# Kernel tuning notes

Hardware: AMD Instinct MI355X
Metric: run time of the kernel (lower is better)

Reference implementation:

```python
import jax, jax.numpy as jnp
import numpy as np

BL = 5
N = 2 ** BL  # 32; LUT is (N+1) x (N+1)


def setup_inputs() -> dict:
    key = jax.random.key(0)
    k1, k2, k3 = jax.random.split(key, 3)
    M, K, O = 512, 256, 256
    x = jax.random.uniform(k1, (M, K), dtype=jnp.float32)              # activations in [0,1)
    W = jax.random.uniform(k2, (O, K), dtype=jnp.float32) * 2.0 - 1.0  # weights in [-1,1)
    b = jax.random.uniform(k3, (O,), dtype=jnp.float32) * 2.0 - 1.0
    # Stochastic-computing multiplication LUT: A[i, j] ~ i*j/N (floored), i,j in [0, N]
    i = np.arange(N + 1, dtype=np.float32)
    lut = jnp.asarray(np.floor(np.outer(i, i) / N), dtype=jnp.float32)
    return {"x": x, "W": W, "b": b, "lut": lut}


def _sanitize(t):
    t = jnp.where(jnp.isnan(t), jnp.zeros_like(t), t)
    return jnp.where(jnp.isinf(t), jnp.ones_like(t), t)


def sc_mat_mac_p(a, b, c, lut, n):
    # Faithful port of SC_MAT_MAC_p: quantize -> LUT gather over all (row, out) pairs ->
    # sign-correct -> reduce over K -> requantize -> add quantized bias -> rescale.
    a = _sanitize(a)
    b = _sanitize(b)
    c = _sanitize(c)
    amax = jnp.abs(a).max()
    amax = jnp.where(amax == 0, jnp.ones_like(amax), amax)
    dmax = jnp.maximum(jnp.abs(b).max(), jnp.abs(c).max())
    dmax = jnp.where(dmax == 0, jnp.ones_like(dmax), dmax)
    # SBL2 = int(log2(int(N / amax))); SN2 = 2**SBL2 (truncations match torch int())
    sn2 = 2.0 ** jnp.floor(jnp.log2(jnp.floor(n / amax)))
    sn1 = 2.0 ** jnp.floor(jnp.log2(jnp.floor(n / dmax)))
    aa = (a * sn2).astype(jnp.int32)  # [M, K], |aa| <= N
    bb = (b * sn1).astype(jnp.int32)  # [O, K], |bb| <= N
    cc = (c * sn1).astype(jnp.int32)  # [O]
    # LUT gather over the full cross product (original materializes this via
    # repeat_interleave/repeat; here it is a broadcasted gather of shape [M, O, K]).
    prod = lut[jnp.abs(aa)[:, None, :], jnp.abs(bb)[None, :, :]]          # [M, O, K]
    sgn = (jnp.sign(aa)[:, None, :] * jnp.sign(bb)[None, :, :]).astype(prod.dtype)
    x9 = (sgn * prod).sum(axis=-1)                                        # [M, O]
    d = (x9 / sn2).astype(jnp.int32) + cc[None, :]
    return d.astype(jnp.float32) / sn1


def reference(x, W, b, lut):
    # out = linear(x); out.data = SC_MAT_MAC_p(...)  -> value is the SC result,
    # gradient path is the dense linear (straight-through via .data assignment).
    lin = x @ W.T + b
    p = sc_mat_mac_p(x, W, b, lut, N)
    return lin + jax.lax.stop_gradient(p - lin)
```

## Files before the change

kernel.cpp:

```cpp
#include <hip/hip_runtime.h>
#include <stdint.h>


#define MROWS 512
#define KDIM  256
#define OCOLS 256
#define E2_GUESS 5
#define E1_GUESS 5

__device__ __forceinline__ void store_uc(unsigned int* p, unsigned int v) {
    asm volatile("global_store_dword %0, %1, off sc0 sc1"
                 :: "v"((unsigned long long)(uintptr_t)p), "v"(v) : "memory");
}
__device__ __forceinline__ unsigned int load_uc(const unsigned int* p) {
    unsigned int v;
    asm volatile("global_load_dword %0, %1, off sc0 sc1\n\t"
                 "s_waitcnt vmcnt(0)"
                 : "=v"(v) : "v"((unsigned long long)(uintptr_t)p) : "memory");
    return v;
}

__device__ __forceinline__ void get_scales(float amax, float dmax, int& e2, int& e1) {
    if (amax == 0.0f) amax = 1.0f;
    if (dmax == 0.0f) dmax = 1.0f;
    float q2 = 32.0f / amax;
    float q1 = 32.0f / dmax;
    int f2 = (q2 >= 1073741824.0f) ? 0x40000000 : (int)floorf(q2);
    int f1 = (q1 >= 1073741824.0f) ? 0x40000000 : (int)floorf(q1);
    if (f2 < 1) f2 = 1;
    if (f1 < 1) f1 = 1;
    e2 = 31 - __clz(f2);
    e1 = 31 - __clz(f1);
}

__device__ __forceinline__ float max4(float4 v) {
    return fmaxf(fmaxf(fabsf(v.x), fabsf(v.y)), fmaxf(fabsf(v.z), fabsf(v.w)));
}

__device__ __forceinline__ void quant_row(const float* __restrict__ x, int m, int o,
                                          float sn2f, unsigned int* a_sh) {
    if (o < KDIM / 4) {
        float4 xv = ((const float4*)(x + (size_t)m * KDIM))[o];
        int a0 = (int)(xv.x * sn2f) & 0xFF;
        int a1 = (int)(xv.y * sn2f) & 0xFF;
        int a2 = (int)(xv.z * sn2f) & 0xFF;
        int a3 = (int)(xv.w * sn2f) & 0xFF;
        a_sh[o] = (unsigned int)(a0 | (a1 << 8) | (a2 << 16) | (a3 << 24));
    }
}

__device__ __forceinline__ int mac_loop(const float* __restrict__ W, int o,
                                        const unsigned int* a_sh, float sn1f) {
    const float4* wrow = (const float4*)(W + (size_t)o * KDIM);
    int sum = 0;
    #pragma unroll 8
    for (int kk = 0; kk < KDIM / 4; ++kk) {
        float4 wv = wrow[kk];
        unsigned int ap = a_sh[kk];
        float wfv[4] = {wv.x, wv.y, wv.z, wv.w};
        #pragma unroll
        for (int j = 0; j < 4; ++j) {
            int bv = (int)(wfv[j] * sn1f);
            int av = ((int)(ap << (24 - 8 * j))) >> 24;
            int s  = av * bv;
            sum += (s + ((s >> 31) & 31)) >> 5;
        }
    }
    return sum;
}

__global__ __launch_bounds__(256, 2)
void k_one(unsigned int* __restrict__ wsp, const float* __restrict__ x,
           const float* __restrict__ W, const float* __restrict__ b,
           float* __restrict__ out) {
    __shared__ unsigned int a_sh[KDIM / 4];
    __shared__ float sm[8];
    __shared__ int s_e[2];

    const int m = blockIdx.x;
    const int o = threadIdx.x;
    const int wave = o >> 6;

    if (m < 64) {
        const float4* xf = (const float4*)x;
        const float4* wf = (const float4*)W;
        float va = fmaxf(max4(xf[m * 512 + o]), max4(xf[m * 512 + 256 + o]));
        float vd = max4(wf[m * 256 + o]);
        if (m == 0 && o < 64)
            vd = fmaxf(vd, max4(((const float4*)b)[o]));
        #pragma unroll
        for (int s = 32; s >= 1; s >>= 1) {
            va = fmaxf(va, __shfl_xor(va, s, 64));
            vd = fmaxf(vd, __shfl_xor(vd, s, 64));
        }
        if ((o & 63) == 0) { sm[2 * wave] = va; sm[2 * wave + 1] = vd; }
        __syncthreads();
        if (o == 0) {
            float a = fmaxf(fmaxf(sm[0], sm[2]), fmaxf(sm[4], sm[6]));
            float d = fmaxf(fmaxf(sm[1], sm[3]), fmaxf(sm[5], sm[7]));
            store_uc(&wsp[2 * m],     __float_as_uint(a));
            store_uc(&wsp[2 * m + 1], __float_as_uint(d));
        }
        __syncthreads();
    }

    float bo = b[o];
    quant_row(x, m, o, (float)(1 << E2_GUESS), a_sh);
    __syncthreads();
    int sum = mac_loop(W, o, a_sh, (float)(1 << E1_GUESS));

    if (wave == 0) {
        unsigned int w0, w1;
        bool all;
        do {
            w0 = load_uc(&wsp[2 * o]);
            w1 = load_uc(&wsp[2 * o + 1]);
            all = __all(((w0 | w1) & 0x80000000u) == 0u);
            if (!all) __builtin_amdgcn_s_sleep(1);
        } while (!all);
        float va = __uint_as_float(w0);
        float vd = __uint_as_float(w1);
        #pragma unroll
        for (int s = 32; s >= 1; s >>= 1) {
            va = fmaxf(va, __shfl_xor(va, s, 64));
            vd = fmaxf(vd, __shfl_xor(vd, s, 64));
        }
        if (o == 0) {
            int e2, e1;
            get_scales(va, vd, e2, e1);
            s_e[0] = e2; s_e[1] = e1;
        }
    }
    __syncthreads();

    const int e2 = s_e[0];
    const int e1 = s_e[1];

    if ((e2 != E2_GUESS) | (e1 != E1_GUESS)) {
        quant_row(x, m, o, (float)(1 << e2), a_sh);
        __syncthreads();
        sum = mac_loop(W, o, a_sh, (float)(1 << e1));
    }

    const float sn1f = (float)(1 << e1);
    int cc = (int)(bo * sn1f);
    int d  = ((sum + ((sum >> 31) & ((1 << e2) - 1))) >> e2) + cc;
    out[(size_t)m * OCOLS + o] = (float)d * (1.0f / sn1f);
}

extern "C" void kernel_launch(void* const* d_in, const int* in_sizes, int n_in,
                              void* d_out, int out_size, void* d_ws, size_t ws_size,
                              hipStream_t stream) {
    const float* x = (const float*)d_in[0];
    const float* W = (const float*)d_in[1];
    const float* b = (const float*)d_in[2];
    float* out = (float*)d_out;
    unsigned int* wsp = (unsigned int*)d_ws;

    k_one<<<MROWS, 256, 0, stream>>>(wsp, x, W, b, out);
}
```

Baseline: 74.71 us.

## Split fused kernel into separate scale-reduction and main MAC kernels

Replaces the single kernel, which spun on uncached workspace flags and speculatively ran the MAC with guessed scales, with two launches: a 64-block max-reduction kernel and a main kernel that reads the finished scales and runs the MAC once. This removes the cross-block spin-wait and the possible redundant recompute. It adds a second kernel launch and its launch gap, and drops the overlap of the speculative MAC with the reduction. The launch-bounds occupancy hint of 2 is also removed.

```diff
diff --git a/kernel.cpp b/kernel.cpp
--- a/kernel.cpp
+++ b/kernel.cpp
@@ -5,20 +5,6 @@
 #define MROWS 512
 #define KDIM  256
 #define OCOLS 256
-#define E2_GUESS 5
-#define E1_GUESS 5
-
-__device__ __forceinline__ void store_uc(unsigned int* p, unsigned int v) {
-    asm volatile("global_store_dword %0, %1, off sc0 sc1"
-                 :: "v"((unsigned long long)(uintptr_t)p), "v"(v) : "memory");
-}
-__device__ __forceinline__ unsigned int load_uc(const unsigned int* p) {
-    unsigned int v;
-    asm volatile("global_load_dword %0, %1, off sc0 sc1\n\t"
-                 "s_waitcnt vmcnt(0)"
-                 : "=v"(v) : "v"((unsigned long long)(uintptr_t)p) : "memory");
-    return v;
-}
 
 __device__ __forceinline__ void get_scales(float amax, float dmax, int& e2, int& e1) {
     if (amax == 0.0f) amax = 1.0f;
@@ -35,18 +21,6 @@
 
 __device__ __forceinline__ float max4(float4 v) {
     return fmaxf(fmaxf(fabsf(v.x), fabsf(v.y)), fmaxf(fabsf(v.z), fabsf(v.w)));
-}
-
-__device__ __forceinline__ void quant_row(const float* __restrict__ x, int m, int o,
-                                          float sn2f, unsigned int* a_sh) {
-    if (o < KDIM / 4) {
-        float4 xv = ((const float4*)(x + (size_t)m * KDIM))[o];
-        int a0 = (int)(xv.x * sn2f) & 0xFF;
-        int a1 = (int)(xv.y * sn2f) & 0xFF;
-        int a2 = (int)(xv.z * sn2f) & 0xFF;
-        int a3 = (int)(xv.w * sn2f) & 0xFF;
-        a_sh[o] = (unsigned int)(a0 | (a1 << 8) | (a2 << 16) | (a3 << 24));
-    }
 }
 
 __device__ __forceinline__ int mac_loop(const float* __restrict__ W, int o,
@@ -69,57 +43,53 @@
     return sum;
 }
 
-__global__ __launch_bounds__(256, 2)
-void k_one(unsigned int* __restrict__ wsp, const float* __restrict__ x,
-           const float* __restrict__ W, const float* __restrict__ b,
-           float* __restrict__ out) {
+__global__ __launch_bounds__(256)
+void k_scales(unsigned int* __restrict__ wsp, const float* __restrict__ x,
+              const float* __restrict__ W, const float* __restrict__ b) {
+    __shared__ float sm[8];
+    const int m = blockIdx.x;
+    const int o = threadIdx.x;
+    const int wave = o >> 6;
+
+    const float4* xf = (const float4*)x;
+    const float4* wf = (const float4*)W;
+    float va = fmaxf(max4(xf[m * 512 + o]), max4(xf[m * 512 + 256 + o]));
+    float vd = max4(wf[m * 256 + o]);
+    if (m == 0 && o < 64)
+        vd = fmaxf(vd, max4(((const float4*)b)[o]));
+    #pragma unroll
+    for (int s = 32; s >= 1; s >>= 1) {
+        va = fmaxf(va, __shfl_xor(va, s, 64));
+        vd = fmaxf(vd, __shfl_xor(vd, s, 64));
+    }
+    if ((o & 63) == 0) { sm[2 * wave] = va; sm[2 * wave + 1] = vd; }
+    __syncthreads();
+    if (o == 0) {
+        float a = fmaxf(fmaxf(sm[0], sm[2]), fmaxf(sm[4], sm[6]));
+        float d = fmaxf(fmaxf(sm[1], sm[3]), fmaxf(sm[5], sm[7]));
+        wsp[2 * m]     = __float_as_uint(a);
+        wsp[2 * m + 1] = __float_as_uint(d);
+    }
+}
+
+__global__ __launch_bounds__(256)
+void k_main(const unsigned int* __restrict__ wsp, const float* __restrict__ x,
+            const float* __restrict__ W, const float* __restrict__ b,
+            float* __restrict__ out) {
     __shared__ unsigned int a_sh[KDIM / 4];
-    __shared__ float sm[8];
     __shared__ int s_e[2];
 
     const int m = blockIdx.x;
     const int o = threadIdx.x;
-    const int wave = o >> 6;
-
-    if (m < 64) {
-        const float4* xf = (const float4*)x;
-        const float4* wf = (const float4*)W;
-        float va = fmaxf(max4(xf[m * 512 + o]), max4(xf[m * 512 + 256 + o]));
-        float vd = max4(wf[m * 256 + o]);
-        if (m == 0 && o < 64)
-            vd = fmaxf(vd, max4(((const float4*)b)[o]));
-        #pragma unroll
-        for (int s = 32; s >= 1; s >>= 1) {
-            va = fmaxf(va, __shfl_xor(va, s, 64));
-            vd = fmaxf(vd, __shfl_xor(vd, s, 64));
-        }
-        if ((o & 63) == 0) { sm[2 * wave] = va; sm[2 * wave + 1] = vd; }
-        __syncthreads();
-        if (o == 0) {
-            float a = fmaxf(fmaxf(sm[0], sm[2]), fmaxf(sm[4], sm[6]));
-            float d = fmaxf(fmaxf(sm[1], sm[3]), fmaxf(sm[5], sm[7]));
-            store_uc(&wsp[2 * m],     __float_as_uint(a));
-            store_uc(&wsp[2 * m + 1], __float_as_uint(d));
-        }
-        __syncthreads();
-    }
 
     float bo = b[o];
-    quant_row(x, m, o, (float)(1 << E2_GUESS), a_sh);
-    __syncthreads();
-    int sum = mac_loop(W, o, a_sh, (float)(1 << E1_GUESS));
+    float4 xv;
+    if (o < KDIM / 4)
+        xv = ((const float4*)(x + (size_t)m * KDIM))[o];
 
-    if (wave == 0) {
-        unsigned int w0, w1;
-        bool all;
-        do {
-            w0 = load_uc(&wsp[2 * o]);
-            w1 = load_uc(&wsp[2 * o + 1]);
-            all = __all(((w0 | w1) & 0x80000000u) == 0u);
-            if (!all) __builtin_amdgcn_s_sleep(1);
-        } while (!all);
-        float va = __uint_as_float(w0);
-        float vd = __uint_as_float(w1);
+    if (o < 64) {
+        float va = __uint_as_float(wsp[2 * o]);
+        float vd = __uint_as_float(wsp[2 * o + 1]);
         #pragma unroll
         for (int s = 32; s >= 1; s >>= 1) {
             va = fmaxf(va, __shfl_xor(va, s, 64));
@@ -135,14 +105,20 @@
 
     const int e2 = s_e[0];
     const int e1 = s_e[1];
+    const float sn2f = (float)(1 << e2);
+    const float sn1f = (float)(1 << e1);
 
-    if ((e2 != E2_GUESS) | (e1 != E1_GUESS)) {
-        quant_row(x, m, o, (float)(1 << e2), a_sh);
-        __syncthreads();
-        sum = mac_loop(W, o, a_sh, (float)(1 << e1));
+    if (o < KDIM / 4) {
+        int a0 = (int)(xv.x * sn2f) & 0xFF;
+        int a1 = (int)(xv.y * sn2f) & 0xFF;
+        int a2 = (int)(xv.z * sn2f) & 0xFF;
+        int a3 = (int)(xv.w * sn2f) & 0xFF;
+        a_sh[o] = (unsigned int)(a0 | (a1 << 8) | (a2 << 16) | (a3 << 24));
     }
+    __syncthreads();
 
-    const float sn1f = (float)(1 << e1);
+    int sum = mac_loop(W, o, a_sh, sn1f);
+
     int cc = (int)(bo * sn1f);
     int d  = ((sum + ((sum >> 31) & ((1 << e2) - 1))) >> e2) + cc;
     out[(size_t)m * OCOLS + o] = (float)d * (1.0f / sn1f);
@@ -157,5 +133,6 @@
     float* out = (float*)d_out;
     unsigned int* wsp = (unsigned int*)d_ws;
 
-    k_one<<<MROWS, 256, 0, stream>>>(wsp, x, W, b, out);
+    k_scales<<<64,    256, 0, stream>>>(wsp, x, W, b);
+    k_main  <<<MROWS, 256, 0, stream>>>(wsp, x, W, b, out);
 }
```

Result: slower. 76.77 us (+2.8%).
